# Performance work log

Measured on AMD Instinct MI355X. Metric: run time of the kernel, lower is better.

Reference implementation:

```python
import jax, jax.numpy as jnp
import numpy as np

N_POINTS = 2_000_000
IN_CH = 10
OUT_CH = 32  # out_channels // 2 since last_layer=False
NUM_PILLARS = 30_000
BN_EPS = 1e-3


def setup_inputs() -> dict:
    key = jax.random.key(0)
    k1, k2, k3, k4, k5 = jax.random.split(key, 5)
    inputs = jax.random.normal(k1, (N_POINTS, IN_CH), dtype=jnp.float32)
    unq_inv = jnp.sort(jax.random.randint(k2, (N_POINTS,), 0, NUM_PILLARS, dtype=jnp.int64))
    W = jax.random.normal(k3, (OUT_CH, IN_CH), dtype=jnp.float32) * 0.1
    gamma = jax.random.uniform(k4, (OUT_CH,), dtype=jnp.float32, minval=0.5, maxval=1.5)
    beta = jax.random.normal(k5, (OUT_CH,), dtype=jnp.float32) * 0.1
    running_mean = jnp.zeros((OUT_CH,), dtype=jnp.float32)
    running_var = jnp.ones((OUT_CH,), dtype=jnp.float32)
    return {
        "inputs": inputs,
        "unq_inv": unq_inv,
        "num_out_inds": NUM_PILLARS,
        "W": W,
        "gamma": gamma,
        "beta": beta,
        "running_mean": running_mean,
        "running_var": running_var,
    }


def reference(inputs, unq_inv, num_out_inds, W, gamma, beta, running_mean, running_var):
    # linear (no bias): [N, in] x [out, in]^T -> [N, out]
    x = jnp.einsum("ni,oi->no", inputs, W)
    # BatchNorm1d (eval / running stats), eps=1e-3
    inv_std = jax.lax.rsqrt(running_var + BN_EPS)
    x = (x - running_mean) * (inv_std * gamma) + beta
    x = jax.nn.relu(x)
    # scatter_max into a zero-initialized buffer: since x >= 0 post-ReLU,
    # this equals max(segment_max, 0); empty segments stay 0.
    x_max = jax.ops.segment_max(x, unq_inv, num_segments=num_out_inds)
    x_max = jnp.maximum(x_max, 0.0)
    # gather back per point and concat -> [N, 2*out]
    return jnp.concatenate([x, x_max[unq_inv, :]], axis=1)
```

## Files before the change

kernel.cpp:

```cpp
#include <hip/hip_runtime.h>

#define IN_CH       10
#define OUT_CH      32
#define NUM_PILLARS 30000
#define BN_EPS      1e-3f

#define BLOCK 256
#define PPB   7
#define CHUNK 512

typedef float fv4 __attribute__((ext_vector_type(4)));
typedef float fv2 __attribute__((ext_vector_type(2)));

__global__ void k_start(const int* __restrict__ inv, int* __restrict__ ps, int n) {
    const int p = blockIdx.x * blockDim.x + threadIdx.x;
    if (p >= n) return;
    const int b = inv[p];
    const int a = (p == 0) ? -1 : inv[p - 1];
    for (int pid = a + 1; pid <= b; ++pid) ps[pid] = p;
    if (p == n - 1)
        for (int pid = b + 1; pid <= NUM_PILLARS; ++pid) ps[pid] = n;
}

__global__ __launch_bounds__(BLOCK) void k_pillar(
    const float* __restrict__ in,
    const int*   __restrict__ inv,
    const float* __restrict__ W,
    const float* __restrict__ gamma,
    const float* __restrict__ beta,
    const float* __restrict__ mean,
    const float* __restrict__ var,
    const int*   __restrict__ ps,
    float*       __restrict__ out,
    int n)
{
    __shared__ float s_sc[OUT_CH], s_b[OUT_CH];
    __shared__ float s_Wf[OUT_CH * IN_CH];
    __shared__ float s_in[CHUNK * 16];
    __shared__ int   s_pid[CHUNK];
    __shared__ unsigned s_pm[PPB * OUT_CH];

    const int t = threadIdx.x;
    const int P0 = blockIdx.x * PPB;
    const int P1 = min(P0 + PPB, NUM_PILLARS);

    if (t < OUT_CH) {
        float sc = rsqrtf(var[t] + BN_EPS) * gamma[t];
        s_sc[t] = sc;
        s_b[t]  = beta[t] - mean[t] * sc;
    }
    if (t < PPB * OUT_CH) s_pm[t] = 0u;
    __syncthreads();
    for (int i = t; i < OUT_CH * IN_CH; i += BLOCK)
        s_Wf[i] = W[i] * s_sc[i / IN_CH];
    __syncthreads();

    const int start = ps[P0];
    const int end   = ps[P1];

    const int strip = t >> 3;
    const int c0 = (t & 7) * 4;
    const int sb = strip & 3;
    const int cslot = t & 15;
    const int pquad = t >> 4;

    float w0[IN_CH], w1[IN_CH], w2[IN_CH], w3[IN_CH];
    #pragma unroll
    for (int i = 0; i < IN_CH; ++i) {
        w0[i] = s_Wf[(c0 + 0) * IN_CH + i];
        w1[i] = s_Wf[(c0 + 1) * IN_CH + i];
        w2[i] = s_Wf[(c0 + 2) * IN_CH + i];
        w3[i] = s_Wf[(c0 + 3) * IN_CH + i];
    }
    const float b0 = s_b[c0], b1 = s_b[c0 + 1], b2 = s_b[c0 + 2], b3 = s_b[c0 + 3];

    for (int cbase = start; cbase < end; cbase += CHUNK) {
        const int cnt = min(CHUNK, end - cbase);
        __syncthreads();
        #pragma unroll
        for (int k = 0; k < (CHUNK * IN_CH) / (BLOCK * 2); ++k) {
            const int f = (t + k * BLOCK) * 2;
            fv2 v = {0.f, 0.f};
            if (f < cnt * IN_CH)
                v = *reinterpret_cast<const fv2*>(in + (long)cbase * IN_CH + f);
            const int r = f / IN_CH, c = f - r * IN_CH;
            const int sw = ((c >> 2) ^ ((r >> 4) & 3)) << 2;
            s_in[r * 16 + sw + (c & 3)]     = v.x;
            s_in[r * 16 + sw + (c & 3) + 1] = v.y;
        }
        #pragma unroll
        for (int k = 0; k < CHUNK / BLOCK; ++k) {
            const int pl = t + k * BLOCK;
            s_pid[pl] = (pl < cnt) ? inv[cbase + pl] : -1;
        }
        __syncthreads();

        int curPid = -1;
        float m0 = 0.f, m1 = 0.f, m2 = 0.f, m3 = 0.f;
        #pragma unroll
        for (int s = 0; s < 16; ++s) {
            const int pl = strip * 16 + s;
            if (pl < cnt) {
                const int pid = s_pid[pl];
                const fv4 x0 = *reinterpret_cast<const fv4*>(&s_in[pl * 16 + ((0 ^ sb) << 2)]);
                const fv4 x1 = *reinterpret_cast<const fv4*>(&s_in[pl * 16 + ((1 ^ sb) << 2)]);
                const fv2 x2 = *reinterpret_cast<const fv2*>(&s_in[pl * 16 + ((2 ^ sb) << 2)]);
                const float xi[IN_CH] = {x0[0], x0[1], x0[2], x0[3],
                                         x1[0], x1[1], x1[2], x1[3], x2[0], x2[1]};
                float a0 = b0, a1 = b1, a2 = b2, a3 = b3;
                #pragma unroll
                for (int i = 0; i < IN_CH; ++i) {
                    a0 = fmaf(xi[i], w0[i], a0);
                    a1 = fmaf(xi[i], w1[i], a1);
                    a2 = fmaf(xi[i], w2[i], a2);
                    a3 = fmaf(xi[i], w3[i], a3);
                }
                a0 = fmaxf(a0, 0.f); a1 = fmaxf(a1, 0.f);
                a2 = fmaxf(a2, 0.f); a3 = fmaxf(a3, 0.f);
                if (pid != curPid) {
                    if (curPid >= 0) {
                        unsigned* q = &s_pm[(curPid - P0) * OUT_CH + c0];
                        atomicMax(q + 0, __float_as_uint(m0));
                        atomicMax(q + 1, __float_as_uint(m1));
                        atomicMax(q + 2, __float_as_uint(m2));
                        atomicMax(q + 3, __float_as_uint(m3));
                    }
                    curPid = pid;
                    m0 = a0; m1 = a1; m2 = a2; m3 = a3;
                } else {
                    m0 = fmaxf(m0, a0); m1 = fmaxf(m1, a1);
                    m2 = fmaxf(m2, a2); m3 = fmaxf(m3, a3);
                }
            }
        }
        if (curPid >= 0) {
            unsigned* q = &s_pm[(curPid - P0) * OUT_CH + c0];
            atomicMax(q + 0, __float_as_uint(m0));
            atomicMax(q + 1, __float_as_uint(m1));
            atomicMax(q + 2, __float_as_uint(m2));
            atomicMax(q + 3, __float_as_uint(m3));
        }
    }
    __syncthreads();

    for (int cbase = start; cbase < end; cbase += CHUNK) {
        const int cnt = min(CHUNK, end - cbase);
        __syncthreads();
        #pragma unroll
        for (int k = 0; k < (CHUNK * IN_CH) / (BLOCK * 2); ++k) {
            const int f = (t + k * BLOCK) * 2;
            fv2 v = {0.f, 0.f};
            if (f < cnt * IN_CH)
                v = *reinterpret_cast<const fv2*>(in + (long)cbase * IN_CH + f);
            const int r = f / IN_CH, c = f - r * IN_CH;
            const int sw = ((c >> 2) ^ ((r >> 4) & 3)) << 2;
            s_in[r * 16 + sw + (c & 3)]     = v.x;
            s_in[r * 16 + sw + (c & 3) + 1] = v.y;
        }
        #pragma unroll
        for (int k = 0; k < CHUNK / BLOCK; ++k) {
            const int pl = t + k * BLOCK;
            s_pid[pl] = (pl < cnt) ? inv[cbase + pl] : P0;
        }
        __syncthreads();

        #pragma unroll 4
        for (int it = 0; it < CHUNK / 16; ++it) {
            const int pl = it * 16 + pquad;
            if (pl < cnt) {
                fv4 v;
                if (cslot < 8) {
                    const int sbB = (pl >> 4) & 3;
                    const fv4 x0 = *reinterpret_cast<const fv4*>(&s_in[pl * 16 + ((0 ^ sbB) << 2)]);
                    const fv4 x1 = *reinterpret_cast<const fv4*>(&s_in[pl * 16 + ((1 ^ sbB) << 2)]);
                    const fv2 x2 = *reinterpret_cast<const fv2*>(&s_in[pl * 16 + ((2 ^ sbB) << 2)]);
                    const float xi[IN_CH] = {x0[0], x0[1], x0[2], x0[3],
                                             x1[0], x1[1], x1[2], x1[3], x2[0], x2[1]};
                    float a0 = b0, a1 = b1, a2 = b2, a3 = b3;
                    #pragma unroll
                    for (int i = 0; i < IN_CH; ++i) {
                        a0 = fmaf(xi[i], w0[i], a0);
                        a1 = fmaf(xi[i], w1[i], a1);
                        a2 = fmaf(xi[i], w2[i], a2);
                        a3 = fmaf(xi[i], w3[i], a3);
                    }
                    v[0] = fmaxf(a0, 0.f); v[1] = fmaxf(a1, 0.f);
                    v[2] = fmaxf(a2, 0.f); v[3] = fmaxf(a3, 0.f);
                } else {
                    const int lp = s_pid[pl] - P0;
                    v = *reinterpret_cast<const fv4*>(&s_pm[lp * OUT_CH + c0]);
                }
                __builtin_nontemporal_store(v,
                    reinterpret_cast<fv4*>(out + (size_t)(cbase + pl) * 64 + cslot * 4));
            }
        }
    }
}

extern "C" void kernel_launch(void* const* d_in, const int* in_sizes, int n_in,
                              void* d_out, int out_size, void* d_ws, size_t ws_size,
                              hipStream_t stream) {
    const float* in    = (const float*)d_in[0];
    const int*   inv   = (const int*)d_in[1];
    const float* W     = (const float*)d_in[3];
    const float* gamma = (const float*)d_in[4];
    const float* beta  = (const float*)d_in[5];
    const float* mean  = (const float*)d_in[6];
    const float* var   = (const float*)d_in[7];
    float* out = (float*)d_out;
    int*   ps  = (int*)d_ws;

    const int n = in_sizes[1];

    k_start<<<(n + BLOCK - 1) / BLOCK, BLOCK, 0, stream>>>(inv, ps, n);

    const int nblk = (NUM_PILLARS + PPB - 1) / PPB;
    k_pillar<<<nblk, BLOCK, 0, stream>>>(in, inv, W, gamma, beta, mean, var,
                                         ps, out, n);
}
```

Measured before the change: 134.3 us.

## Store linear outputs in first pass and drop input reload in second pass

The first pass now writes the ReLU'd linear result for each point directly to the first half of the output row as it computes it. The second pass no longer reloads inputs into shared memory or recomputes the matmul. It only reads pillar ids from global memory and writes the per-pillar max to the second half of each row. This removes a full second read of the input and the redundant FMAs. In exchange the first-pass stores are 16-byte pieces of 256-byte rows, so write coalescing is worse.

```diff
diff --git a/kernel.cpp b/kernel.cpp
--- a/kernel.cpp
+++ b/kernel.cpp
@@ -61,8 +61,6 @@
     const int strip = t >> 3;
     const int c0 = (t & 7) * 4;
     const int sb = strip & 3;
-    const int cslot = t & 15;
-    const int pquad = t >> 4;
 
     float w0[IN_CH], w1[IN_CH], w2[IN_CH], w3[IN_CH];
     #pragma unroll
@@ -117,6 +115,11 @@
                 }
                 a0 = fmaxf(a0, 0.f); a1 = fmaxf(a1, 0.f);
                 a2 = fmaxf(a2, 0.f); a3 = fmaxf(a3, 0.f);
+
+                fv4 v = {a0, a1, a2, a3};
+                __builtin_nontemporal_store(v,
+                    reinterpret_cast<fv4*>(out + (size_t)(cbase + pl) * 64 + c0));
+
                 if (pid != curPid) {
                     if (curPid >= 0) {
                         unsigned* q = &s_pm[(curPid - P0) * OUT_CH + c0];
@@ -143,55 +146,17 @@
     }
     __syncthreads();
 
+    const int slot8 = t & 7;
+    const int pofs  = t >> 3;
     for (int cbase = start; cbase < end; cbase += CHUNK) {
         const int cnt = min(CHUNK, end - cbase);
-        __syncthreads();
-        #pragma unroll
-        for (int k = 0; k < (CHUNK * IN_CH) / (BLOCK * 2); ++k) {
-            const int f = (t + k * BLOCK) * 2;
-            fv2 v = {0.f, 0.f};
-            if (f < cnt * IN_CH)
-                v = *reinterpret_cast<const fv2*>(in + (long)cbase * IN_CH + f);
-            const int r = f / IN_CH, c = f - r * IN_CH;
-            const int sw = ((c >> 2) ^ ((r >> 4) & 3)) << 2;
-            s_in[r * 16 + sw + (c & 3)]     = v.x;
-            s_in[r * 16 + sw + (c & 3) + 1] = v.y;
-        }
-        #pragma unroll
-        for (int k = 0; k < CHUNK / BLOCK; ++k) {
-            const int pl = t + k * BLOCK;
-            s_pid[pl] = (pl < cnt) ? inv[cbase + pl] : P0;
-        }
-        __syncthreads();
-
-        #pragma unroll 4
-        for (int it = 0; it < CHUNK / 16; ++it) {
-            const int pl = it * 16 + pquad;
+        for (int it = 0; it < CHUNK / 32; ++it) {
+            const int pl = it * 32 + pofs;
             if (pl < cnt) {
-                fv4 v;
-                if (cslot < 8) {
-                    const int sbB = (pl >> 4) & 3;
-                    const fv4 x0 = *reinterpret_cast<const fv4*>(&s_in[pl * 16 + ((0 ^ sbB) << 2)]);
-                    const fv4 x1 = *reinterpret_cast<const fv4*>(&s_in[pl * 16 + ((1 ^ sbB) << 2)]);
-                    const fv2 x2 = *reinterpret_cast<const fv2*>(&s_in[pl * 16 + ((2 ^ sbB) << 2)]);
-                    const float xi[IN_CH] = {x0[0], x0[1], x0[2], x0[3],
-                                             x1[0], x1[1], x1[2], x1[3], x2[0], x2[1]};
-                    float a0 = b0, a1 = b1, a2 = b2, a3 = b3;
-                    #pragma unroll
-                    for (int i = 0; i < IN_CH; ++i) {
-                        a0 = fmaf(xi[i], w0[i], a0);
-                        a1 = fmaf(xi[i], w1[i], a1);
-                        a2 = fmaf(xi[i], w2[i], a2);
-                        a3 = fmaf(xi[i], w3[i], a3);
-                    }
-                    v[0] = fmaxf(a0, 0.f); v[1] = fmaxf(a1, 0.f);
-                    v[2] = fmaxf(a2, 0.f); v[3] = fmaxf(a3, 0.f);
-                } else {
-                    const int lp = s_pid[pl] - P0;
-                    v = *reinterpret_cast<const fv4*>(&s_pm[lp * OUT_CH + c0]);
-                }
+                const int lp = inv[cbase + pl] - P0;
+                fv4 v = *reinterpret_cast<const fv4*>(&s_pm[lp * OUT_CH + slot8 * 4]);
                 __builtin_nontemporal_store(v,
-                    reinterpret_cast<fv4*>(out + (size_t)(cbase + pl) * 64 + cslot * 4));
+                    reinterpret_cast<fv4*>(out + (size_t)(cbase + pl) * 64 + 32 + slot8 * 4));
             }
         }
     }
```

After: 111.6 us. 16.9% less time.
